# Optimization experiments

Hardware: AMD Instinct MI355X
Metric: run time of the kernel (lower is better)

## Reference

```python
import jax, jax.numpy as jnp
import numpy as np

THETA = 10000.0

def _rope(x, cos, sin):
    # x: [B, S, D]; cos/sin: [S, D/2]. Pairs are (x[..., 2i], x[..., 2i+1]) treated as complex.
    xr = x.reshape(*x.shape[:-1], -1, 2)
    x0, x1 = xr[..., 0], xr[..., 1]
    o0 = x0 * cos - x1 * sin
    o1 = x0 * sin + x1 * cos
    return jnp.stack([o0, o1], axis=-1).reshape(x.shape)

def setup_inputs() -> dict:
    key = jax.random.key(0)
    ks = jax.random.split(key, 7)
    B, S, D = 4, 2048, 1024
    sd = 1.0 / np.sqrt(D)
    return {
        "x": jax.random.normal(ks[0], (B, S, D), dtype=jnp.float32),
        "wq_w": jax.random.normal(ks[1], (D, D), dtype=jnp.float32) * sd,
        "wq_b": jax.random.normal(ks[2], (D,), dtype=jnp.float32) * 0.01,
        "wk_w": jax.random.normal(ks[3], (D, D), dtype=jnp.float32) * sd,
        "wk_b": jax.random.normal(ks[4], (D,), dtype=jnp.float32) * 0.01,
        "wv_w": jax.random.normal(ks[5], (D, D), dtype=jnp.float32) * sd,
        "wv_b": jax.random.normal(ks[6], (D,), dtype=jnp.float32) * 0.01,
    }

def reference(x, wq_w, wq_b, wk_w, wk_b, wv_w, wv_b):
    B, S, D = x.shape
    # QKV projections (torch Linear: y = x @ W.T + b)
    q = jnp.einsum('bsd,ed->bse', x, wq_w) + wq_b
    k = jnp.einsum('bsd,ed->bse', x, wk_w) + wk_b
    v = jnp.einsum('bsd,ed->bse', x, wv_w) + wv_b
    # Rotary embedding: freqs_cis[t, i] = exp(i * t / theta^(2i/D))
    inv_freq = 1.0 / (THETA ** (jnp.arange(0, D, 2, dtype=jnp.float32) / D))  # [D/2]
    ang = jnp.arange(S, dtype=jnp.float32)[:, None] * inv_freq[None, :]  # [S, D/2]
    cos, sin = jnp.cos(ang), jnp.sin(ang)
    q = _rope(q, cos, sin)
    k = _rope(k, cos, sin)
    # Full (non-causal, single-head) attention with scale 1/sqrt(dim)
    scores = jnp.einsum('bqd,bkd->bqk', q, k) / jnp.sqrt(jnp.float32(D))
    probs = jax.nn.softmax(scores.astype(jnp.float32), axis=-1)
    return jnp.einsum('bqk,bkd->bqd', probs, v)
```

## Files before the change

kernel.cpp:

```cpp
#include <hip/hip_runtime.h>
#include <cstdint>

using u16 = unsigned short;
using u32 = unsigned int;

typedef __attribute__((ext_vector_type(8))) short short8;
typedef __attribute__((ext_vector_type(4))) float floatx4;

__device__ __forceinline__ u16 f2bf(float f) {
    u32 u = __float_as_uint(f);
    u32 r = u + 0x7fffu + ((u >> 16) & 1u);
    return (u16)(r >> 16);
}

__global__ void cvt_all(const float* __restrict__ x, u16* __restrict__ xb,
                        const float* __restrict__ w0, const float* __restrict__ w1,
                        const float* __restrict__ w2,
                        u16* __restrict__ o0, u16* __restrict__ o1, u16* __restrict__ o2,
                        const float* __restrict__ qb, const float* __restrict__ kb,
                        float* __restrict__ bqk, float* __restrict__ rowsum)
{
    int b = blockIdx.x;
    if (b >= 11272) {
        long i = ((long)(b - 11272) * 256 + threadIdx.x) * 4;
        *reinterpret_cast<float4*>(rowsum + i) = make_float4(0.f, 0.f, 0.f, 0.f);
        return;
    }
    if (b >= 11264) {
        int i = (b - 11264) * 256 + threadIdx.x;
        bqk[i] = (i < 1024) ? qb[i] : kb[i - 1024];
        return;
    }
    const float* src; u16* dst; long base;
    if (b < 8192) { src = x; dst = xb; base = (long)b; }
    else {
        int r = b - 8192, seg = r >> 10;
        if (seg == 0)      { src = w0; dst = o0; }
        else if (seg == 1) { src = w1; dst = o1; }
        else               { src = w2; dst = o2; }
        base = (long)(r & 1023);
    }
    long i = (base * 256 + threadIdx.x) * 4;
    float4 v = *reinterpret_cast<const float4*>(src + i);
    uint2 o;
    o.x = (u32)f2bf(v.x) | ((u32)f2bf(v.y) << 16);
    o.y = (u32)f2bf(v.z) | ((u32)f2bf(v.w) << 16);
    *reinterpret_cast<uint2*>(dst + i) = o;
}

__device__ __forceinline__ void async_cp16(const u16* g, u16* l) {
    __builtin_amdgcn_global_load_lds(
        (const __attribute__((address_space(1))) void*)g,
        (__attribute__((address_space(3))) void*)l, 16, 0, 0);
}

#define MEMFENCE asm volatile("" ::: "memory")
__device__ __forceinline__ void barrier_raw() {
    MEMFENCE; __builtin_amdgcn_s_barrier(); MEMFENCE;
}
__device__ __forceinline__ void vmwait(int n) {
    if      (n == 6) asm volatile("s_waitcnt vmcnt(6)" ::: "memory");
    else if (n == 4) asm volatile("s_waitcnt vmcnt(4)" ::: "memory");
    else if (n == 2) asm volatile("s_waitcnt vmcnt(2)" ::: "memory");
    else if (n == 0) asm volatile("s_waitcnt vmcnt(0)" ::: "memory");
}

template <bool BF16_OUT, bool EXPOUT>
__device__ __forceinline__ void gemm_core(
    const u16* __restrict__ A, const u16* __restrict__ B, void* __restrict__ Cv,
    int K, int lda, int ldb, int ldc,
    long tile_m, long tile_n, long cbase,
    const float* bias_col, const float* bias_row,
    float scale, bool rope, float* __restrict__ rowsum,
    const float* __restrict__ rowscale, u16* smem)
{
    u16* As = smem;
    u16* Bs = smem + 8192;

    const int tid  = threadIdx.x;
    const int lane = tid & 63;
    const int wave = tid >> 6;
    const int wm = (wave >> 1) << 6;
    const int wn = (wave & 1) << 6;

    floatx4 acc[4][4] = {};

    const int srow = tid >> 2;
    const int skp  = (((tid & 3) ^ (srow & 3))) * 8;
    const u16* Ag = A + (tile_m + srow) * (long)lda + skp;
    const u16* Bg = B + (tile_n + srow) * (long)ldb + skp;
    u16* Asl = &As[tid * 8];
    u16* Bsl = &Bs[tid * 8];

    const int fm  = lane & 15;
    const int fks = (((lane >> 4) ^ (lane & 3))) * 8;

    for (int k0 = 0; k0 < K; k0 += 64) {
        async_cp16(Ag,                       Asl);
        async_cp16(Ag + 64 * (long)lda,      Asl + 64 * 32);
        async_cp16(Ag + 32,                  Asl + 4096);
        async_cp16(Ag + 32 + 64 * (long)lda, Asl + 4096 + 64 * 32);
        async_cp16(Bg,                       Bsl);
        async_cp16(Bg + 64 * (long)ldb,      Bsl + 64 * 32);
        async_cp16(Bg + 32,                  Bsl + 4096);
        async_cp16(Bg + 32 + 64 * (long)ldb, Bsl + 4096 + 64 * 32);
        Ag += 64; Bg += 64;
        __syncthreads();

        #pragma unroll
        for (int c = 0; c < 2; ++c) {
            const u16* Ap = As + c * 4096;
            const u16* Bp = Bs + c * 4096;
            short8 af[4], bfr[4];
            #pragma unroll
            for (int i = 0; i < 4; ++i)
                af[i] = *reinterpret_cast<const short8*>(&Ap[(wm + i * 16 + fm) * 32 + fks]);
            #pragma unroll
            for (int j = 0; j < 4; ++j)
                bfr[j] = *reinterpret_cast<const short8*>(&Bp[(wn + j * 16 + fm) * 32 + fks]);
            #pragma unroll
            for (int i = 0; i < 4; ++i)
                #pragma unroll
                for (int j = 0; j < 4; ++j)
                    acc[i][j] = __builtin_amdgcn_mfma_f32_16x16x32_bf16(af[i], bfr[j], acc[i][j], 0, 0, 0);
        }
        __syncthreads();
    }

    const int q4  = lane >> 4;
    const int c16 = lane & 15;
    float* smemf  = (float*)smem;
    float* myeps = smemf + wave * (16 * 68);
    const long n0 = tile_n + wn + c16 * 4;

    float4 bc4 = make_float4(0.f, 0.f, 0.f, 0.f);
    if (bias_col) bc4 = *reinterpret_cast<const float4*>(bias_col + n0);

    float inv0 = 0.f, inv1 = 0.f;
    if (rope) {
        int p0 = (int)(n0 >> 1);
        inv0 = __expf((float)(p0 & 511)       * -1.79889463e-2f);
        inv1 = __expf((float)((p0 + 1) & 511) * -1.79889463e-2f);
    }

    #pragma unroll
    for (int i = 0; i < 4; ++i) {
        #pragma unroll
        for (int j = 0; j < 4; ++j)
            #pragma unroll
            for (int r = 0; r < 4; ++r)
                myeps[(q4 * 4 + r) * 68 + j * 16 + c16] = acc[i][j][r];
        __syncthreads();
        #pragma unroll
        for (int p = 0; p < 4; ++p) {
            int lrow = p * 4 + q4;
            long m = tile_m + wm + i * 16 + lrow;
            float4 v = *reinterpret_cast<const float4*>(&myeps[lrow * 68 + c16 * 4]);
            float sc = scale;
            if (rowscale) sc *= 1.0f / rowscale[m];
            v.x = v.x * sc + bc4.x;
            v.y = v.y * sc + bc4.y;
            v.z = v.z * sc + bc4.z;
            v.w = v.w * sc + bc4.w;
            if (bias_row) {
                float br = bias_row[m];
                v.x += br; v.y += br; v.z += br; v.w += br;
            }
            if (rope) {
                int s = (int)(m & 2047);
                float a0 = (float)s * inv0, a1 = (float)s * inv1;
                float sn0 = __sinf(a0), cs0 = __cosf(a0);
                float sn1 = __sinf(a1), cs1 = __cosf(a1);
                float x0 = v.x, x1 = v.y, x2 = v.z, x3 = v.w;
                v.x = x0 * cs0 - x1 * sn0;
                v.y = x0 * sn0 + x1 * cs0;
                v.z = x2 * cs1 - x3 * sn1;
                v.w = x2 * sn1 + x3 * cs1;
            }
            if constexpr (EXPOUT) {
                v.x = __expf(v.x); v.y = __expf(v.y);
                v.z = __expf(v.z); v.w = __expf(v.w);
                float s4 = v.x + v.y + v.z + v.w;
                s4 += __shfl_xor(s4, 1);
                s4 += __shfl_xor(s4, 2);
                s4 += __shfl_xor(s4, 4);
                s4 += __shfl_xor(s4, 8);
                if (c16 == 0) atomicAdd(&rowsum[m], s4);
            }
            long off = cbase + m * (long)ldc + n0;
            if constexpr (BF16_OUT) {
                uint2 o;
                o.x = (u32)f2bf(v.x) | ((u32)f2bf(v.y) << 16);
                o.y = (u32)f2bf(v.z) | ((u32)f2bf(v.w) << 16);
                *reinterpret_cast<uint2*>((u16*)Cv + off) = o;
            } else {
                *reinterpret_cast<float4*>((float*)Cv + off) = v;
            }
        }
        __syncthreads();
    }
}

template <bool BF16_OUT, bool EXPOUT>
__device__ __forceinline__ void gemm8_core(
    const u16* __restrict__ A, const u16* __restrict__ B, void* __restrict__ Cv,
    int K, int lda, int ldb, int ldc,
    long tile_m, long tile_n, long cbase,
    const float* __restrict__ bias_col, const float* __restrict__ bias_row,
    float scale, bool rope, float* __restrict__ rowsum, u16* smem)
{
    const int tid  = threadIdx.x;
    const int lane = tid & 63;
    const int wave = tid >> 6;
    const int wm2  = (wave >> 2) * 128;
    const int wn2  = (wave & 3) * 64;
    const int fm   = lane & 15;
    const int fks  = (((lane >> 4) ^ ((lane >> 1) & 3))) * 8;

    const int srow = tid >> 2;
    const int kgl  = ((tid & 3) ^ ((tid >> 3) & 3)) * 8;
    const u16* Asrc = A + (tile_m + srow) * (long)lda + kgl;
    const u16* Bsrc = B + (tile_n + srow) * (long)ldb + kgl;
    u16* dst0 = smem + tid * 8;

    const int U = K >> 5;

    floatx4 acc[8][4] = {};
    short8 bf[4];

    auto stageA = [&](int v) {
        u16* d = dst0 + ((2 * v) & 7) * 8192;
        const u16* s = Asrc + v * 32;
        async_cp16(s, d);
        async_cp16(s + 128 * (long)lda, d + 4096);
    };
    auto stageB = [&](int v) {
        u16* d = dst0 + ((2 * v + 1) & 7) * 8192;
        const u16* s = Bsrc + v * 32;
        async_cp16(s, d);
        async_cp16(s + 128 * (long)ldb, d + 4096);
    };

    auto phase_pair = [&](int u, int vmx, bool stb, bool sta)
        __attribute__((always_inline))
    {
        const u16* Ap = smem + ((2 * u) & 7) * 8192;
        const u16* Bp = smem + ((2 * u + 1) & 7) * 8192;
        short8 af[4];
        #pragma unroll
        for (int i = 0; i < 4; ++i)
            af[i] = *reinterpret_cast<const short8*>(&Ap[(wm2 + i * 16 + fm) * 32 + fks]);
        #pragma unroll
        for (int j = 0; j < 4; ++j)
            bf[j] = *reinterpret_cast<const short8*>(&Bp[(wn2 + j * 16 + fm) * 32 + fks]);
        if (stb) stageB(u + 2);
        vmwait(vmx);
        barrier_raw();
        __builtin_amdgcn_sched_barrier(0);
        __builtin_amdgcn_s_setprio(1);
        #pragma unroll
        for (int i = 0; i < 4; ++i)
            #pragma unroll
            for (int j = 0; j < 4; ++j)
                acc[i][j] = __builtin_amdgcn_mfma_f32_16x16x32_bf16(af[i], bf[j], acc[i][j], 0, 0, 0);
        __builtin_amdgcn_s_setprio(0);
        __builtin_amdgcn_sched_barrier(0);
        barrier_raw();
        #pragma unroll
        for (int i = 0; i < 4; ++i)
            af[i] = *reinterpret_cast<const short8*>(&Ap[(wm2 + 64 + i * 16 + fm) * 32 + fks]);
        if (sta) stageA(u + 3);
        barrier_raw();
        __builtin_amdgcn_sched_barrier(0);
        __builtin_amdgcn_s_setprio(1);
        #pragma unroll
        for (int i = 0; i < 4; ++i)
            #pragma unroll
            for (int j = 0; j < 4; ++j)
                acc[4 + i][j] = __builtin_amdgcn_mfma_f32_16x16x32_bf16(af[i], bf[j], acc[4 + i][j], 0, 0, 0);
        __builtin_amdgcn_s_setprio(0);
        __builtin_amdgcn_sched_barrier(0);
        barrier_raw();
    };

    stageA(0); stageB(0); stageA(1); stageB(1); stageA(2);
    vmwait(6);
    barrier_raw();

    for (int u = 0; u + 3 < U; ++u)
        phase_pair(u, 6, true, true);
    phase_pair(U - 3, 6, true,  false);
    phase_pair(U - 2, 2, false, false);
    phase_pair(U - 1, 0, false, false);

    const int q4  = lane >> 4;
    const int c16 = lane & 15;
    float* smemf  = (float*)smem;
    float* myeps  = smemf + wave * (16 * 68);
    const long n0 = tile_n + wn2 + c16 * 4;

    float4 bc4 = make_float4(0.f, 0.f, 0.f, 0.f);
    if (bias_col) bc4 = *reinterpret_cast<const float4*>(bias_col + n0);

    float inv0 = 0.f, inv1 = 0.f;
    if (rope) {
        int p0 = (int)(n0 >> 1);
        inv0 = __expf((float)(p0 & 511)       * -1.79889463e-2f);
        inv1 = __expf((float)((p0 + 1) & 511) * -1.79889463e-2f);
    }

    #pragma unroll
    for (int i = 0; i < 8; ++i) {
        #pragma unroll
        for (int j = 0; j < 4; ++j)
            #pragma unroll
            for (int r = 0; r < 4; ++r)
                myeps[(q4 * 4 + r) * 68 + j * 16 + c16] = acc[i][j][r];
        __syncthreads();
        #pragma unroll
        for (int p = 0; p < 4; ++p) {
            int lrow = p * 4 + q4;
            long m = tile_m + wm2 + i * 16 + lrow;
            float4 v = *reinterpret_cast<const float4*>(&myeps[lrow * 68 + c16 * 4]);
            v.x = v.x * scale + bc4.x;
            v.y = v.y * scale + bc4.y;
            v.z = v.z * scale + bc4.z;
            v.w = v.w * scale + bc4.w;
            if (bias_row) {
                float br = bias_row[m];
                v.x += br; v.y += br; v.z += br; v.w += br;
            }
            if (rope) {
                int s = (int)(m & 2047);
                float a0 = (float)s * inv0, a1 = (float)s * inv1;
                float sn0 = __sinf(a0), cs0 = __cosf(a0);
                float sn1 = __sinf(a1), cs1 = __cosf(a1);
                float x0 = v.x, x1 = v.y, x2 = v.z, x3 = v.w;
                v.x = x0 * cs0 - x1 * sn0;
                v.y = x0 * sn0 + x1 * cs0;
                v.z = x2 * cs1 - x3 * sn1;
                v.w = x2 * sn1 + x3 * cs1;
            }
            if constexpr (EXPOUT) {
                v.x = __expf(v.x); v.y = __expf(v.y);
                v.z = __expf(v.z); v.w = __expf(v.w);
                float s4 = v.x + v.y + v.z + v.w;
                s4 += __shfl_xor(s4, 1);
                s4 += __shfl_xor(s4, 2);
                s4 += __shfl_xor(s4, 4);
                s4 += __shfl_xor(s4, 8);
                if (c16 == 0) atomicAdd(&rowsum[m], s4);
            }
            long off = cbase + m * (long)ldc + n0;
            if constexpr (BF16_OUT) {
                uint2 o;
                o.x = (u32)f2bf(v.x) | ((u32)f2bf(v.y) << 16);
                o.y = (u32)f2bf(v.z) | ((u32)f2bf(v.w) << 16);
                *reinterpret_cast<uint2*>((u16*)Cv + off) = o;
            } else {
                *reinterpret_cast<float4*>((float*)Cv + off) = v;
            }
        }
        __syncthreads();
    }
}

__global__ __launch_bounds__(256, 4)
void gemm_fused12(const u16* __restrict__ xb, const u16* __restrict__ wqk,
                  const u16* __restrict__ wv, u16* __restrict__ QK, u16* __restrict__ VT,
                  const float* __restrict__ bqk, const float* __restrict__ wvb)
{
    u32 id = blockIdx.x;
    id = (id & 7u) * 192u + (id >> 3);
    __shared__ alignas(16) u16 smem[16384];
    if (id < 1024u) {
        u32 bx = id & 15u, by = id >> 4;
        gemm_core<true, false>(xb, wqk, QK, 1024, 1024, 1024, 2048,
                        (long)by * 128, (long)bx * 128, 0L,
                        bqk, nullptr, 1.0f, true, nullptr, nullptr, smem);
    } else {
        u32 r = id - 1024u;
        u32 bx = r & 15u, by = (r >> 4) & 7u, bz = r >> 7;
        gemm_core<true, false>(wv, xb + (long)bz * 2048 * 1024, VT,
                        1024, 1024, 1024, 2048,
                        (long)by * 128, (long)bx * 128, (long)bz * 1024 * 2048,
                        nullptr, wvb, 1.0f, false, nullptr, nullptr, smem);
    }
}

__global__ __launch_bounds__(512, 2)
void gemm8_qkt(const u16* __restrict__ QK, u16* __restrict__ Pbuf,
               float* __restrict__ rsum)
{
    u32 id = blockIdx.x;
    id = (id & 7u) * 32u + (id >> 3);
    u32 bz = id >> 6, q = id & 63u, bx = q & 7u, by = q >> 3;
    __shared__ alignas(16) u16 smem[65536];
    const u16* base = QK + (long)bz * 2048 * 2048;
    gemm8_core<true, true>(base, base + 1024, Pbuf, 1024, 2048, 2048, 2048,
                           (long)by * 256, (long)bx * 256, (long)bz * 2048 * 2048,
                           nullptr, nullptr, 0.03125f, false,
                           rsum + (long)bz * 2048, smem);
}

template <bool BF16_OUT, bool EXPOUT>
__global__ __launch_bounds__(256, 4)
void gemm_nt(const u16* __restrict__ A, const u16* __restrict__ B, void* __restrict__ Cv,
             int K, int lda, int ldb, int ldc,
             long sA, long sB, long sC,
             const float* __restrict__ bias_col, const float* __restrict__ bias_row,
             float scale, float* __restrict__ rowsum, const float* __restrict__ rowscale)
{
    const u32 gx = gridDim.x, gy = gridDim.y;
    u32 id = blockIdx.x + gx * (blockIdx.y + gy * blockIdx.z);
    const u32 G = gx * gy * gridDim.z;
    if ((G & 7u) == 0u) id = (id & 7u) * (G >> 3) + (id >> 3);
    const u32 bx = id % gx;
    const u32 t1 = id / gx;
    const u32 by = t1 % gy;
    const u32 bz = t1 / gy;

    __shared__ alignas(16) u16 smem[16384];
    gemm_core<BF16_OUT, EXPOUT>(A + (long)bz * sA, B + (long)bz * sB, Cv,
                        K, lda, ldb, ldc,
                        (long)by * 128, (long)bx * 128, (long)bz * sC,
                        bias_col, bias_row, scale, false,
                        rowsum ? rowsum + (long)bz * 2048 : nullptr,
                        rowscale ? rowscale + (long)bz * 2048 : nullptr, smem);
}

extern "C" void kernel_launch(void* const* d_in, const int* in_sizes, int n_in,
                              void* d_out, int out_size, void* d_ws, size_t ws_size,
                              hipStream_t stream)
{
    const float* x   = (const float*)d_in[0];
    const float* wqw = (const float*)d_in[1];
    const float* wqb = (const float*)d_in[2];
    const float* wkw = (const float*)d_in[3];
    const float* wkb = (const float*)d_in[4];
    const float* wvw = (const float*)d_in[5];
    const float* wvb = (const float*)d_in[6];
    float* out = (float*)d_out;

    char* ws = (char*)d_ws;
    const size_t MB = 1ull << 20;
    u16*   Pbuf = (u16*)(ws + 64 * MB);
    u16*   QK   = (u16*)(ws + 96 * MB);
    u16*   VT   = (u16*)(ws + 128 * MB);
    float* rsum = (float*)(ws + 144 * MB);
    u16*   xb    = (u16*)(ws + 0);
    u16*   wqk   = (u16*)(ws + 16 * MB);
    u16*   wvbuf = (u16*)(ws + 20 * MB);
    float* bqk   = (float*)(ws + 22 * MB);

    cvt_all<<<dim3(11280), 256, 0, stream>>>(x, xb, wqw, wkw, wvw,
                                             wqk, wqk + 1024 * 1024, wvbuf,
                                             wqb, wkb, bqk, rsum);

    gemm_fused12<<<dim3(1536), 256, 0, stream>>>(xb, wqk, wvbuf, QK, VT, bqk, wvb);

    gemm8_qkt<<<dim3(256), 512, 0, stream>>>(QK, Pbuf, rsum);

    gemm_nt<false, false><<<dim3(8, 16, 4), 256, 0, stream>>>(
        Pbuf, VT, out, 2048, 2048, 2048, 1024,
        2048L * 2048, 1024L * 2048, 2048L * 1024,
        nullptr, nullptr, 1.0f, nullptr, rsum);

    (void)in_sizes; (void)n_in; (void)out_size; (void)ws_size;
}
```

Before: 236.6 us.

## Move 256x256 pipelined GEMM from QK^T to PV with 256x128 tiles

The large 8-wave pipelined GEMM core is specialised into a 256x128-tile variant with a smaller B stage and ring buffer, and used for the P·V product, which now normalises by the row sums in its epilogue. The QK^T product falls back to the generic 128x128 gemm_nt with exp output and row-sum atomics. The aim is to give PV, which has a long K of 2048, the deeper-reuse kernel, at the cost of a less efficient QK^T kernel. The vmcnt wait counts are adjusted to match the new number of async copies per stage.

```diff
diff --git a/kernel.cpp b/kernel.cpp
--- a/kernel.cpp
+++ b/kernel.cpp
@@ -59,9 +59,8 @@
     MEMFENCE; __builtin_amdgcn_s_barrier(); MEMFENCE;
 }
 __device__ __forceinline__ void vmwait(int n) {
-    if      (n == 6) asm volatile("s_waitcnt vmcnt(6)" ::: "memory");
-    else if (n == 4) asm volatile("s_waitcnt vmcnt(4)" ::: "memory");
-    else if (n == 2) asm volatile("s_waitcnt vmcnt(2)" ::: "memory");
+    if      (n == 5) asm volatile("s_waitcnt vmcnt(5)" ::: "memory");
+    else if (n == 3) asm volatile("s_waitcnt vmcnt(3)" ::: "memory");
     else if (n == 0) asm volatile("s_waitcnt vmcnt(0)" ::: "memory");
 }
 
@@ -201,19 +200,17 @@
     }
 }
 
-template <bool BF16_OUT, bool EXPOUT>
-__device__ __forceinline__ void gemm8_core(
-    const u16* __restrict__ A, const u16* __restrict__ B, void* __restrict__ Cv,
+__device__ __forceinline__ void gemm8n128_core(
+    const u16* __restrict__ A, const u16* __restrict__ B, float* __restrict__ C,
     int K, int lda, int ldb, int ldc,
     long tile_m, long tile_n, long cbase,
-    const float* __restrict__ bias_col, const float* __restrict__ bias_row,
-    float scale, bool rope, float* __restrict__ rowsum, u16* smem)
+    const float* __restrict__ rowscale, u16* smem)
 {
     const int tid  = threadIdx.x;
     const int lane = tid & 63;
     const int wave = tid >> 6;
     const int wm2  = (wave >> 2) * 128;
-    const int wn2  = (wave & 3) * 64;
+    const int wn2  = (wave & 3) * 32;
     const int fm   = lane & 15;
     const int fks  = (((lane >> 4) ^ ((lane >> 1) & 3))) * 8;
 
@@ -225,33 +222,30 @@
 
     const int U = K >> 5;
 
-    floatx4 acc[8][4] = {};
-    short8 bf[4];
+    floatx4 acc[8][2] = {};
+    short8 bf[2];
 
     auto stageA = [&](int v) {
-        u16* d = dst0 + ((2 * v) & 7) * 8192;
+        u16* d = dst0 + (v & 3) * 12288;
         const u16* s = Asrc + v * 32;
         async_cp16(s, d);
         async_cp16(s + 128 * (long)lda, d + 4096);
     };
     auto stageB = [&](int v) {
-        u16* d = dst0 + ((2 * v + 1) & 7) * 8192;
-        const u16* s = Bsrc + v * 32;
-        async_cp16(s, d);
-        async_cp16(s + 128 * (long)ldb, d + 4096);
+        async_cp16(Bsrc + v * 32, dst0 + (v & 3) * 12288 + 8192);
     };
 
     auto phase_pair = [&](int u, int vmx, bool stb, bool sta)
         __attribute__((always_inline))
     {
-        const u16* Ap = smem + ((2 * u) & 7) * 8192;
-        const u16* Bp = smem + ((2 * u + 1) & 7) * 8192;
+        const u16* Ap = smem + (u & 3) * 12288;
+        const u16* Bp = Ap + 8192;
         short8 af[4];
         #pragma unroll
         for (int i = 0; i < 4; ++i)
             af[i] = *reinterpret_cast<const short8*>(&Ap[(wm2 + i * 16 + fm) * 32 + fks]);
         #pragma unroll
-        for (int j = 0; j < 4; ++j)
+        for (int j = 0; j < 2; ++j)
             bf[j] = *reinterpret_cast<const short8*>(&Bp[(wn2 + j * 16 + fm) * 32 + fks]);
         if (stb) stageB(u + 2);
         vmwait(vmx);
@@ -261,7 +255,7 @@
         #pragma unroll
         for (int i = 0; i < 4; ++i)
             #pragma unroll
-            for (int j = 0; j < 4; ++j)
+            for (int j = 0; j < 2; ++j)
                 acc[i][j] = __builtin_amdgcn_mfma_f32_16x16x32_bf16(af[i], bf[j], acc[i][j], 0, 0, 0);
         __builtin_amdgcn_s_setprio(0);
         __builtin_amdgcn_sched_barrier(0);
@@ -276,7 +270,7 @@
         #pragma unroll
         for (int i = 0; i < 4; ++i)
             #pragma unroll
-            for (int j = 0; j < 4; ++j)
+            for (int j = 0; j < 2; ++j)
                 acc[4 + i][j] = __builtin_amdgcn_mfma_f32_16x16x32_bf16(af[i], bf[j], acc[4 + i][j], 0, 0, 0);
         __builtin_amdgcn_s_setprio(0);
         __builtin_amdgcn_sched_barrier(0);
@@ -284,82 +278,37 @@
     };
 
     stageA(0); stageB(0); stageA(1); stageB(1); stageA(2);
-    vmwait(6);
+    vmwait(5);
     barrier_raw();
 
     for (int u = 0; u + 3 < U; ++u)
-        phase_pair(u, 6, true, true);
-    phase_pair(U - 3, 6, true,  false);
-    phase_pair(U - 2, 2, false, false);
+        phase_pair(u, 3, true, true);
+    phase_pair(U - 3, 3, true,  false);
+    phase_pair(U - 2, 0, false, false);
     phase_pair(U - 1, 0, false, false);
 
     const int q4  = lane >> 4;
     const int c16 = lane & 15;
-    float* smemf  = (float*)smem;
-    float* myeps  = smemf + wave * (16 * 68);
-    const long n0 = tile_n + wn2 + c16 * 4;
-
-    float4 bc4 = make_float4(0.f, 0.f, 0.f, 0.f);
-    if (bias_col) bc4 = *reinterpret_cast<const float4*>(bias_col + n0);
-
-    float inv0 = 0.f, inv1 = 0.f;
-    if (rope) {
-        int p0 = (int)(n0 >> 1);
-        inv0 = __expf((float)(p0 & 511)       * -1.79889463e-2f);
-        inv1 = __expf((float)((p0 + 1) & 511) * -1.79889463e-2f);
-    }
+    float* smemf = (float*)smem;
+    float* myeps = smemf + wave * (16 * 36);
+    const long n0 = tile_n + wn2 + c16 * 2;
 
     #pragma unroll
     for (int i = 0; i < 8; ++i) {
         #pragma unroll
-        for (int j = 0; j < 4; ++j)
+        for (int j = 0; j < 2; ++j)
             #pragma unroll
             for (int r = 0; r < 4; ++r)
-                myeps[(q4 * 4 + r) * 68 + j * 16 + c16] = acc[i][j][r];
+                myeps[(q4 * 4 + r) * 36 + j * 16 + c16] = acc[i][j][r];
         __syncthreads();
         #pragma unroll
         for (int p = 0; p < 4; ++p) {
             int lrow = p * 4 + q4;
             long m = tile_m + wm2 + i * 16 + lrow;
-            float4 v = *reinterpret_cast<const float4*>(&myeps[lrow * 68 + c16 * 4]);
-            v.x = v.x * scale + bc4.x;
-            v.y = v.y * scale + bc4.y;
-            v.z = v.z * scale + bc4.z;
-            v.w = v.w * scale + bc4.w;
-            if (bias_row) {
-                float br = bias_row[m];
-                v.x += br; v.y += br; v.z += br; v.w += br;
-            }
-            if (rope) {
-                int s = (int)(m & 2047);
-                float a0 = (float)s * inv0, a1 = (float)s * inv1;
-                float sn0 = __sinf(a0), cs0 = __cosf(a0);
-                float sn1 = __sinf(a1), cs1 = __cosf(a1);
-                float x0 = v.x, x1 = v.y, x2 = v.z, x3 = v.w;
-                v.x = x0 * cs0 - x1 * sn0;
-                v.y = x0 * sn0 + x1 * cs0;
-                v.z = x2 * cs1 - x3 * sn1;
-                v.w = x2 * sn1 + x3 * cs1;
-            }
-            if constexpr (EXPOUT) {
-                v.x = __expf(v.x); v.y = __expf(v.y);
-                v.z = __expf(v.z); v.w = __expf(v.w);
-                float s4 = v.x + v.y + v.z + v.w;
-                s4 += __shfl_xor(s4, 1);
-                s4 += __shfl_xor(s4, 2);
-                s4 += __shfl_xor(s4, 4);
-                s4 += __shfl_xor(s4, 8);
-                if (c16 == 0) atomicAdd(&rowsum[m], s4);
-            }
-            long off = cbase + m * (long)ldc + n0;
-            if constexpr (BF16_OUT) {
-                uint2 o;
-                o.x = (u32)f2bf(v.x) | ((u32)f2bf(v.y) << 16);
-                o.y = (u32)f2bf(v.z) | ((u32)f2bf(v.w) << 16);
-                *reinterpret_cast<uint2*>((u16*)Cv + off) = o;
-            } else {
-                *reinterpret_cast<float4*>((float*)Cv + off) = v;
-            }
+            float2 v = *reinterpret_cast<const float2*>(&myeps[lrow * 36 + c16 * 2]);
+            float sc = 1.0f / rowscale[m];
+            v.x *= sc; v.y *= sc;
+            *reinterpret_cast<float2*>(C + cbase + m * (long)ldc + n0) = v;
         }
         __syncthreads();
     }
@@ -388,21 +337,6 @@
     }
 }
 
-__global__ __launch_bounds__(512, 2)
-void gemm8_qkt(const u16* __restrict__ QK, u16* __restrict__ Pbuf,
-               float* __restrict__ rsum)
-{
-    u32 id = blockIdx.x;
-    id = (id & 7u) * 32u + (id >> 3);
-    u32 bz = id >> 6, q = id & 63u, bx = q & 7u, by = q >> 3;
-    __shared__ alignas(16) u16 smem[65536];
-    const u16* base = QK + (long)bz * 2048 * 2048;
-    gemm8_core<true, true>(base, base + 1024, Pbuf, 1024, 2048, 2048, 2048,
-                           (long)by * 256, (long)bx * 256, (long)bz * 2048 * 2048,
-                           nullptr, nullptr, 0.03125f, false,
-                           rsum + (long)bz * 2048, smem);
-}
-
 template <bool BF16_OUT, bool EXPOUT>
 __global__ __launch_bounds__(256, 4)
 void gemm_nt(const u16* __restrict__ A, const u16* __restrict__ B, void* __restrict__ Cv,
@@ -427,6 +361,21 @@
                         bias_col, bias_row, scale, false,
                         rowsum ? rowsum + (long)bz * 2048 : nullptr,
                         rowscale ? rowscale + (long)bz * 2048 : nullptr, smem);
+}
+
+__global__ __launch_bounds__(512, 2)
+void gemm8_pv(const u16* __restrict__ Pbuf, const u16* __restrict__ VT,
+              float* __restrict__ out, const float* __restrict__ rsum)
+{
+    u32 id = blockIdx.x;
+    id = (id & 7u) * 32u + (id >> 3);
+    u32 bz = id >> 6, q = id & 63u, by = q >> 3, bx = q & 7u;
+    __shared__ alignas(16) u16 smem[49152];
+    gemm8n128_core(Pbuf + (long)bz * 2048 * 2048,
+                   VT   + (long)bz * 1024 * 2048,
+                   out, 2048, 2048, 2048, 1024,
+                   (long)by * 256, (long)bx * 128, (long)bz * 2048 * 1024,
+                   rsum + (long)bz * 2048, smem);
 }
 
 extern "C" void kernel_launch(void* const* d_in, const int* in_sizes, int n_in,
@@ -459,12 +408,12 @@
 
     gemm_fused12<<<dim3(1536), 256, 0, stream>>>(xb, wqk, wvbuf, QK, VT, bqk, wvb);
 
-    gemm8_qkt<<<dim3(256), 512, 0, stream>>>(QK, Pbuf, rsum);
-
-    gemm_nt<false, false><<<dim3(8, 16, 4), 256, 0, stream>>>(
-        Pbuf, VT, out, 2048, 2048, 2048, 1024,
-        2048L * 2048, 1024L * 2048, 2048L * 1024,
-        nullptr, nullptr, 1.0f, nullptr, rsum);
+    gemm_nt<true, true><<<dim3(16, 16, 4), 256, 0, stream>>>(
+        QK, QK + 1024, Pbuf, 1024, 2048, 2048, 2048,
+        2048L * 2048, 2048L * 2048, 2048L * 2048,
+        nullptr, nullptr, 0.03125f, rsum, nullptr);
+
+    gemm8_pv<<<dim3(256), 512, 0, stream>>>(Pbuf, VT, out, rsum);
 
     (void)in_sizes; (void)n_in; (void)out_size; (void)ws_size;
 }
```

Result: slower. 243.1 us (+2.8%).
